# Performance work log

Measured on AMD Instinct MI355X. Metric: run time of the kernel, lower is better.

## Reference

```python
import jax, jax.numpy as jnp
import numpy as np
from jax import lax

B, S, HDIM = 4, 2048, 1024
H, D, L = 16, 64, 128
NB = S // L
EPS = 1e-8


def setup_inputs() -> dict:
    key = jax.random.key(0)
    ks = jax.random.split(key, 16)
    std = 0.02
    inp = {
        'f_in': jax.random.normal(ks[0], (B, S, HDIM), jnp.float32),
        'i_in': jax.random.normal(ks[1], (B, S, HDIM), jnp.float32),
        'z_in': jax.random.normal(ks[2], (B, S, HDIM), jnp.float32),
        'o_in': jax.random.normal(ks[3], (B, S, HDIM), jnp.float32),
        'c0': jax.random.normal(ks[4], (B, H, D), jnp.float32),
        'h0': jax.random.normal(ks[5], (B, H, D), jnp.float32),
        # weights stored (in, out) so forward is x @ W + b
        'Wf': std * jax.random.normal(ks[6], (HDIM, H * D), jnp.float32),
        'bf': jnp.zeros((H * D,), jnp.float32),
        'Wi': std * jax.random.normal(ks[7], (HDIM, H * D), jnp.float32),
        'bi': jnp.zeros((H * D,), jnp.float32),
        'Wz': std * jax.random.normal(ks[8], (HDIM, H * D), jnp.float32),
        'bz': jnp.zeros((H * D,), jnp.float32),
        'Wo': std * jax.random.normal(ks[9], (HDIM, H * D), jnp.float32),
        'bo': jnp.zeros((H * D,), jnp.float32),
        'Wp': std * jax.random.normal(ks[10], (H * D, HDIM), jnp.float32),
        'bp': jnp.zeros((HDIM,), jnp.float32),
    }
    return inp


def _to_blocks(x):
    # (B,S,H*D) -> (NB, B, H, D, L), matching torch view+permute(1,0,3,4,2)
    return jnp.transpose(x.reshape(B, NB, L, H, D), (1, 0, 3, 4, 2))


def _qlstm(f_in, i_in, z_in, o_in, c0, Wf, bf, Wi, bi, Wz, bz, Wo, bo, Wp, bp):
    fx = _to_blocks(f_in @ Wf + bf)
    ix = _to_blocks(i_in @ Wi + bi)
    zx = _to_blocks(z_in @ Wz + bz)
    ox = _to_blocks(o_in @ Wo + bo)

    f = jax.nn.sigmoid(fx + 1.0)              # (NB,B,H,D,L)
    o = jax.nn.sigmoid(ox)
    update = jax.nn.sigmoid(ix) * jnp.tanh(zx)

    kk = jnp.arange(L)[:, None]
    ll = jnp.arange(L + 1)[None, :]
    ones_mask = ll >= kk + 1                   # (L, L+1): filled with 1.0
    zeros_mask = ll >= kk + 2                  # (L, L+1): zeroed out

    def block_step(c, blk):
        fb, ob, ub = blk                       # each (B,H,D,L)
        cf = jnp.concatenate([fb, jnp.ones(fb.shape[:-1] + (1,), fb.dtype)], axis=-1)  # (B,H,D,L+1)
        Fm = jnp.broadcast_to(cf[..., None, :], fb.shape[:-1] + (L, L + 1))
        Fm = jnp.where(ones_mask, 1.0, Fm)
        # reversed log-cumsum-exp along last axis (decay products)
        Fm = jnp.exp(jnp.flip(jnp.cumsum(jnp.flip(jnp.log(Fm + EPS), -1), -1), -1)) - EPS
        Fm = jnp.where(zeros_mask, 0.0, Fm)    # (B,H,D,L,L+1)
        u = jnp.concatenate([c[..., None], ub], axis=-1)   # (B,H,D,L+1)
        cs = jnp.einsum('bhdkl,bhdl->bhdk', Fm, u)          # (B,H,D,L)
        hs = ob * jnp.tanh(cs)
        return cs[..., -1], hs

    last_c, hs = lax.scan(block_step, c0, (f, o, update))   # hs: (NB,B,H,D,L)
    last_h = hs[-1, ..., -1]
    y = jnp.transpose(hs, (1, 0, 4, 2, 3)).reshape(B, S, H * D)
    y = y @ Wp + bp                            # (B,S,HDIM)
    return y, last_c, last_h


def reference(f_in, i_in, z_in, o_in, c0, h0, Wf, bf, Wi, bi, Wz, bz, Wo, bo, Wp, bp):
    y, last_c, last_h = _qlstm(f_in, i_in, z_in, o_in, c0,
                               Wf, bf, Wi, bi, Wz, bz, Wo, bo, Wp, bp)
    return y, last_c, last_h
```

## Files before the change

### kernel.cpp

```cpp
#include <hip/hip_runtime.h>
#include <hip/hip_bf16.h>
#include <stdint.h>

constexpr int GM = 8192;
constexpr int GK = 1024;
constexpr int GN = 1024;
constexpr size_t NACT = (size_t)GM * GN;
constexpr int CHUNK = 32;
constexpr int NCHUNK = 64;
constexpr int NCH = 4096;
constexpr int NT = GK / 64;

#define DEVINL __device__ __forceinline__

typedef __attribute__((ext_vector_type(8))) short bf16x8;
typedef __attribute__((ext_vector_type(4))) float f32x4;

DEVINL float sigmoidf_(float x) { return 1.0f / (1.0f + __expf(-x)); }

DEVINL unsigned short f2bf(float x) {
  unsigned int u = __builtin_bit_cast(unsigned int, x);
  unsigned int rnd = 0x7fffu + ((u >> 16) & 1u);
  return (unsigned short)((u + rnd) >> 16);
}
DEVINL float bf2f(unsigned short u) {
  unsigned int x = ((unsigned int)u) << 16;
  return __builtin_bit_cast(float, x);
}

DEVINL void gload16(const void* g, void* l) {
  __builtin_amdgcn_global_load_lds(
      (const __attribute__((address_space(1))) unsigned int*)g,
      (__attribute__((address_space(3))) unsigned int*)l, 16, 0, 0);
}

__global__ void cvt4_kernel(const float* __restrict__ s0, const float* __restrict__ s1,
                            const float* __restrict__ s2, const float* __restrict__ s3,
                            unsigned short* __restrict__ d0, unsigned short* __restrict__ d1,
                            unsigned short* __restrict__ d2, unsigned short* __restrict__ d3,
                            int n4) {
  const float* s;
  unsigned short* d;
  switch (blockIdx.y) {
    case 0: s = s0; d = d0; break;
    case 1: s = s1; d = d1; break;
    case 2: s = s2; d = d2; break;
    default: s = s3; d = d3; break;
  }
  int stride = gridDim.x * blockDim.x;
  for (int i = blockIdx.x * blockDim.x + threadIdx.x; i < n4; i += stride) {
    float4 v = ((const float4*)s)[i];
    ushort4 o;
    o.x = f2bf(v.x); o.y = f2bf(v.y); o.z = f2bf(v.z); o.w = f2bf(v.w);
    ((ushort4*)d)[i] = o;
  }
}

struct TPtrs {
  const float* src[5];
  unsigned short* dst[5];
};

__global__ void transpose_cvt_all(TPtrs p) {
  const float* __restrict__ W = p.src[blockIdx.z];
  unsigned short* __restrict__ Wt = p.dst[blockIdx.z];
  __shared__ float tile[32][33];
  int n0 = blockIdx.x * 32, k0 = blockIdx.y * 32;
  int tx = threadIdx.x & 31, ty = threadIdx.x >> 5;
#pragma unroll
  for (int i = 0; i < 32; i += 8)
    tile[ty + i][tx] = W[(size_t)(k0 + ty + i) * GN + n0 + tx];
  __syncthreads();
#pragma unroll
  for (int i = 0; i < 32; i += 8)
    Wt[(size_t)(n0 + ty + i) * GK + k0 + tx] = f2bf(tile[tx][ty + i]);
}

DEVINL void gemm256_core(const unsigned short* __restrict__ A,
                         const unsigned short* __restrict__ W,
                         char* lds, int tid, int wave, int lane,
                         int bm, int bn, f32x4 (&acc)[8][4]) {
  const int Ah = wave >> 2;
  const int wn = (wave & 3) * 64;
  const int lrow = lane & 15;
  const int lgrp = lane >> 4;

  const char* gsrc[8];
  char* ldst[8];
  {
    const char* Ag = (const char*)A;
    const char* Wg = (const char*)W;
#pragma unroll
    for (int hh = 0; hh < 4; ++hh)
#pragma unroll
      for (int j = 0; j < 2; ++j) {
        const int lbyte = j * 8192 + tid * 16;
        const int row = lbyte >> 7;
        const int gcb = (lbyte & 127) ^ ((row & 7) << 4);
        const int i = hh * 2 + j;
        gsrc[i] = (hh < 2)
            ? Ag + (size_t)(bm * 256 + hh * 128 + row) * 2048 + gcb
            : Wg + (size_t)(bn * 256 + (hh - 2) * 128 + row) * 2048 + gcb;
        ldst[i] = lds + (hh >= 2 ? 32768 : 0) + (hh & 1) * 16384 + j * 8192 +
                  wave * 1024;
      }
  }

#pragma unroll
  for (int i = 0; i < 8; ++i) gload16(gsrc[i], ldst[i]);

  bf16x8 aF[4][2], bF[4][2];

  for (int t = 0; t < NT; ++t) {
    const int cur = t & 1;
    const int obuf = (cur ^ 1) * 65536;
    const char* Abase = lds + cur * 65536 + Ah * 16384;
    const char* Bbase = lds + cur * 65536 + 32768;
    const int nk = (t + 1 < NT) ? (t + 1) : (NT - 1);
    const size_t koff = (size_t)nk * 128;

#pragma unroll
    for (int i = 0; i < 4; ++i) gload16(gsrc[i] + koff, ldst[i] + obuf);
    asm volatile("s_waitcnt vmcnt(4)" ::: "memory");
    __builtin_amdgcn_s_barrier();
    __builtin_amdgcn_sched_barrier(0);
#pragma unroll
    for (int m = 0; m < 4; ++m)
#pragma unroll
      for (int ks = 0; ks < 2; ++ks) {
        const int r = m * 16 + lrow;
        const int cb = ks * 64 + lgrp * 16;
        aF[m][ks] = *(const bf16x8*)(Abase + r * 128 + (cb ^ ((r & 7) << 4)));
      }
#pragma unroll
    for (int n = 0; n < 2; ++n)
#pragma unroll
      for (int ks = 0; ks < 2; ++ks) {
        const int nr = wn + n * 16 + lrow;
        const int cb = ks * 64 + lgrp * 16;
        bF[n][ks] = *(const bf16x8*)(Bbase + nr * 128 + (cb ^ ((nr & 7) << 4)));
      }
    __builtin_amdgcn_s_setprio(1);
#pragma unroll
    for (int m = 0; m < 4; ++m)
#pragma unroll
      for (int n = 0; n < 2; ++n)
#pragma unroll
        for (int ks = 0; ks < 2; ++ks)
          acc[m][n] = __builtin_amdgcn_mfma_f32_16x16x32_bf16(aF[m][ks], bF[n][ks],
                                                              acc[m][n], 0, 0, 0);
    __builtin_amdgcn_s_setprio(0);

#pragma unroll
    for (int n = 2; n < 4; ++n)
#pragma unroll
      for (int ks = 0; ks < 2; ++ks) {
        const int nr = wn + n * 16 + lrow;
        const int cb = ks * 64 + lgrp * 16;
        bF[n][ks] = *(const bf16x8*)(Bbase + nr * 128 + (cb ^ ((nr & 7) << 4)));
      }
#pragma unroll
    for (int i = 4; i < 8; ++i) gload16(gsrc[i] + koff, ldst[i] + obuf);
    __builtin_amdgcn_s_barrier();
    asm volatile("s_waitcnt lgkmcnt(0)" ::: "memory");
    __builtin_amdgcn_sched_barrier(0);
    __builtin_amdgcn_s_setprio(1);
#pragma unroll
    for (int m = 0; m < 4; ++m)
#pragma unroll
      for (int n = 2; n < 4; ++n)
#pragma unroll
        for (int ks = 0; ks < 2; ++ks)
          acc[m][n] = __builtin_amdgcn_mfma_f32_16x16x32_bf16(aF[m][ks], bF[n][ks],
                                                              acc[m][n], 0, 0, 0);
    __builtin_amdgcn_s_setprio(0);

#pragma unroll
    for (int m = 0; m < 4; ++m)
#pragma unroll
      for (int ks = 0; ks < 2; ++ks) {
        const int r = (m + 4) * 16 + lrow;
        const int cb = ks * 64 + lgrp * 16;
        aF[m][ks] = *(const bf16x8*)(Abase + r * 128 + (cb ^ ((r & 7) << 4)));
      }
    __builtin_amdgcn_s_barrier();
    asm volatile("s_waitcnt lgkmcnt(0)" ::: "memory");
    __builtin_amdgcn_sched_barrier(0);
    __builtin_amdgcn_s_setprio(1);
#pragma unroll
    for (int m = 0; m < 4; ++m)
#pragma unroll
      for (int n = 2; n < 4; ++n)
#pragma unroll
        for (int ks = 0; ks < 2; ++ks)
          acc[m + 4][n] = __builtin_amdgcn_mfma_f32_16x16x32_bf16(aF[m][ks], bF[n][ks],
                                                                  acc[m + 4][n], 0, 0, 0);
    __builtin_amdgcn_s_setprio(0);

    __builtin_amdgcn_s_barrier();
    __builtin_amdgcn_s_setprio(1);
#pragma unroll
    for (int m = 0; m < 4; ++m)
#pragma unroll
      for (int n = 0; n < 2; ++n)
#pragma unroll
        for (int ks = 0; ks < 2; ++ks)
          acc[m + 4][n] = __builtin_amdgcn_mfma_f32_16x16x32_bf16(aF[m][ks], bF[n][ks],
                                                                  acc[m + 4][n], 0, 0, 0);
    __builtin_amdgcn_s_setprio(0);
  }
}

struct GateArgs {
  const unsigned short* A[4];
  const unsigned short* W[4];
  const float* bias[4];
  unsigned short* out[4];
};

__global__ __launch_bounds__(512, 2) void gemm_gates8(GateArgs ga) {
  extern __shared__ char lds[];
  const int tid = threadIdx.x;
  const int wave = tid >> 6, lane = tid & 63;
  const int bm = blockIdx.x, bn = blockIdx.y, gz = blockIdx.z;
  const int wm = (wave >> 2) * 128, wn = (wave & 3) * 64;
  const int lrow = lane & 15, lgrp = lane >> 4;

  f32x4 acc[8][4];
#pragma unroll
  for (int m = 0; m < 8; ++m)
#pragma unroll
    for (int n = 0; n < 4; ++n) acc[m][n] = (f32x4){0.f, 0.f, 0.f, 0.f};

  gemm256_core(ga.A[gz], ga.W[gz], lds, tid, wave, lane, bm, bn, acc);

  const float* bias = ga.bias[gz];
  unsigned short* out = ga.out[gz];
  float bv[4];
#pragma unroll
  for (int n = 0; n < 4; ++n) bv[n] = bias[bn * 256 + wn + n * 16 + lrow];

#pragma unroll
  for (int m = 0; m < 8; ++m)
#pragma unroll
    for (int n = 0; n < 4; ++n) {
      const int gc = bn * 256 + wn + n * 16 + lrow;
#pragma unroll
      for (int j = 0; j < 4; ++j) {
        const int gr = bm * 256 + wm + m * 16 + lgrp * 4 + j;
        float v = acc[m][n][j] + bv[n];
        if (gz == 0) v = sigmoidf_(v + 1.0f);
        else if (gz == 1) v = sigmoidf_(v);
        out[(size_t)gr * GN + gc] = f2bf(v);
      }
    }
}

__global__ __launch_bounds__(512, 2) void gemm_proj8(
    const unsigned short* __restrict__ A, const unsigned short* __restrict__ W,
    const float* __restrict__ bias, float* __restrict__ out) {
  extern __shared__ char lds[];
  const int tid = threadIdx.x;
  const int wave = tid >> 6, lane = tid & 63;
  const int bm = blockIdx.x, bn = blockIdx.y;
  const int wm = (wave >> 2) * 128, wn = (wave & 3) * 64;
  const int lrow = lane & 15, lgrp = lane >> 4;

  f32x4 acc[8][4];
#pragma unroll
  for (int m = 0; m < 8; ++m)
#pragma unroll
    for (int n = 0; n < 4; ++n) acc[m][n] = (f32x4){0.f, 0.f, 0.f, 0.f};

  gemm256_core(A, W, lds, tid, wave, lane, bm, bn, acc);

  float bv[4];
#pragma unroll
  for (int n = 0; n < 4; ++n) bv[n] = bias[bn * 256 + wn + n * 16 + lrow];

#pragma unroll
  for (int m = 0; m < 8; ++m)
#pragma unroll
    for (int n = 0; n < 4; ++n) {
      const int gc = bn * 256 + wn + n * 16 + lrow;
#pragma unroll
      for (int j = 0; j < 4; ++j) {
        const int gr = bm * 256 + wm + m * 16 + lgrp * 4 + j;
        out[(size_t)gr * GN + gc] = acc[m][n][j] + bv[n];
      }
    }
}

__global__ void scan_phaseA_kernel(const unsigned short* __restrict__ F,
                                   const unsigned short* __restrict__ Ip,
                                   const unsigned short* __restrict__ Zp,
                                   float* __restrict__ Pt, float* __restrict__ Ct) {
  int tid = blockIdx.x * blockDim.x + threadIdx.x;
  int ch = tid & (NCH - 1), chunk = tid >> 12;
  int b = ch >> 10, n = ch & 1023;
  size_t base = ((size_t)(b * 2048 + chunk * CHUNK)) * 1024 + n;
  float c = 0.f, P = 1.f;
#pragma unroll 8
  for (int t = 0; t < CHUNK; ++t) {
    size_t idx = base + (size_t)t * 1024;
    float f = bf2f(F[idx]);
    float u = sigmoidf_(bf2f(Ip[idx])) * tanhf(bf2f(Zp[idx]));
    c = __builtin_fmaf(f, c, u);
    P *= f;
  }
  Pt[tid] = P;
  Ct[tid] = c;
}

__global__ void scan_combine_kernel(const float* __restrict__ Pt,
                                    const float* __restrict__ Ct,
                                    const float* __restrict__ c0,
                                    float* __restrict__ Cin,
                                    float* __restrict__ last_c) {
  int ch = blockIdx.x * blockDim.x + threadIdx.x;
  float c = c0[ch];
#pragma unroll
  for (int j = 0; j < NCHUNK; ++j) {
    Cin[j * NCH + ch] = c;
    c = __builtin_fmaf(Pt[j * NCH + ch], c, Ct[j * NCH + ch]);
  }
  last_c[ch] = c;
}

__global__ void scan_phaseC_kernel(const unsigned short* __restrict__ F,
                                   const unsigned short* __restrict__ Ip,
                                   const unsigned short* __restrict__ Zp,
                                   const unsigned short* __restrict__ O,
                                   const float* __restrict__ Cin,
                                   unsigned short* __restrict__ Hb,
                                   float* __restrict__ last_h) {
  int tid = blockIdx.x * blockDim.x + threadIdx.x;
  int ch = tid & (NCH - 1), chunk = tid >> 12;
  int b = ch >> 10, n = ch & 1023;
  size_t base = ((size_t)(b * 2048 + chunk * CHUNK)) * 1024 + n;
  float c = Cin[tid];
  float h = 0.f;
#pragma unroll 8
  for (int t = 0; t < CHUNK; ++t) {
    size_t idx = base + (size_t)t * 1024;
    float f = bf2f(F[idx]);
    float u = sigmoidf_(bf2f(Ip[idx])) * tanhf(bf2f(Zp[idx]));
    float o = bf2f(O[idx]);
    c = __builtin_fmaf(f, c, u);
    h = o * tanhf(c);
    Hb[idx] = f2bf(h);
  }
  if (chunk == NCHUNK - 1) last_h[ch] = h;
}

extern "C" void kernel_launch(void* const* d_in, const int* in_sizes, int n_in,
                              void* d_out, int out_size, void* d_ws, size_t ws_size,
                              hipStream_t stream) {
  const float* f_in = (const float*)d_in[0];
  const float* i_in = (const float*)d_in[1];
  const float* z_in = (const float*)d_in[2];
  const float* o_in = (const float*)d_in[3];
  const float* c0 = (const float*)d_in[4];
  const float* Wf = (const float*)d_in[6];
  const float* bf_ = (const float*)d_in[7];
  const float* Wi = (const float*)d_in[8];
  const float* bi = (const float*)d_in[9];
  const float* Wz = (const float*)d_in[10];
  const float* bz = (const float*)d_in[11];
  const float* Wo = (const float*)d_in[12];
  const float* bo = (const float*)d_in[13];
  const float* Wp = (const float*)d_in[14];
  const float* bp = (const float*)d_in[15];

  float* y = (float*)d_out;
  float* last_c = y + NACT;
  float* last_h = last_c + NCH;

  char* w = (char*)d_ws;
  const size_t ABYTES = NACT * 2;
  const size_t WBYTES = (size_t)GK * GN * 2;
  unsigned short* Af = (unsigned short*)(w + 0 * ABYTES);
  unsigned short* Ai = (unsigned short*)(w + 1 * ABYTES);
  unsigned short* Az = (unsigned short*)(w + 2 * ABYTES);
  unsigned short* Ao = (unsigned short*)(w + 3 * ABYTES);
  char* wt = w + 4 * ABYTES;
  unsigned short* Wtf = (unsigned short*)(wt + 0 * WBYTES);
  unsigned short* Wti = (unsigned short*)(wt + 1 * WBYTES);
  unsigned short* Wtz = (unsigned short*)(wt + 2 * WBYTES);
  unsigned short* Wto = (unsigned short*)(wt + 3 * WBYTES);
  unsigned short* Wtp = (unsigned short*)(wt + 4 * WBYTES);
  char* gp = wt + 5 * WBYTES;
  unsigned short* F = (unsigned short*)(gp + 0 * ABYTES);
  unsigned short* O = (unsigned short*)(gp + 1 * ABYTES);
  unsigned short* Ip = (unsigned short*)(gp + 2 * ABYTES);
  unsigned short* Zp = (unsigned short*)(gp + 3 * ABYTES);
  unsigned short* Hb = Af;
  char* sp = gp + 4 * ABYTES;
  const size_t SBYTES = (size_t)NCH * NCHUNK * 4;
  float* Pt = (float*)(sp + 0 * SBYTES);
  float* Ct = (float*)(sp + 1 * SBYTES);
  float* Cin = (float*)(sp + 2 * SBYTES);

  (void)hipFuncSetAttribute((const void*)gemm_gates8,
                            hipFuncAttributeMaxDynamicSharedMemorySize, 131072);
  (void)hipFuncSetAttribute((const void*)gemm_proj8,
                            hipFuncAttributeMaxDynamicSharedMemorySize, 131072);

  cvt4_kernel<<<dim3(1024, 4), 256, 0, stream>>>(
      f_in, o_in, i_in, z_in, Af, Ao, Ai, Az, (int)(NACT / 4));

  TPtrs tp;
  tp.src[0] = Wf; tp.src[1] = Wi; tp.src[2] = Wz; tp.src[3] = Wo; tp.src[4] = Wp;
  tp.dst[0] = Wtf; tp.dst[1] = Wti; tp.dst[2] = Wtz; tp.dst[3] = Wto; tp.dst[4] = Wtp;
  transpose_cvt_all<<<dim3(32, 32, 5), 256, 0, stream>>>(tp);

  GateArgs ga;
  ga.A[0] = Af;  ga.A[1] = Ao;  ga.A[2] = Ai;  ga.A[3] = Az;
  ga.W[0] = Wtf; ga.W[1] = Wto; ga.W[2] = Wti; ga.W[3] = Wtz;
  ga.bias[0] = bf_; ga.bias[1] = bo; ga.bias[2] = bi; ga.bias[3] = bz;
  ga.out[0] = F; ga.out[1] = O; ga.out[2] = Ip; ga.out[3] = Zp;
  gemm_gates8<<<dim3(GM / 256, GN / 256, 4), 512, 131072, stream>>>(ga);

  scan_phaseA_kernel<<<(NCH * NCHUNK) / 256, 256, 0, stream>>>(F, Ip, Zp, Pt, Ct);
  scan_combine_kernel<<<NCH / 256, 256, 0, stream>>>(Pt, Ct, c0, Cin, last_c);
  scan_phaseC_kernel<<<(NCH * NCHUNK) / 256, 256, 0, stream>>>(F, Ip, Zp, O, Cin, Hb,
                                                               last_h);

  gemm_proj8<<<dim3(GM / 256, GN / 256), 512, 131072, stream>>>(Hb, Wtp, bp, y);
}
```

Measured before the change: 206.1 us.

## Restructure GEMM mainloop with full fragment registers and one barrier per k-step

Changes the GEMM inner loop from four barrier-separated phases with shared fragment registers to a single barrier per k-tile. All eight async global-to-LDS loads for the next tile are issued right after it. All A/B fragments for the tile are held in separate Lo/Hi registers, with partial lgkmcnt waits so the MFMAs can start while later LDS reads are still in flight. This cuts barrier overhead and lets LDS reads overlap with MFMA work. In exchange it raises register pressure and waits on vmcnt(0), which may expose global load latency at the top of each iteration.

```diff
diff --git a/kernel.cpp b/kernel.cpp
--- a/kernel.cpp
+++ b/kernel.cpp
@@ -33,6 +33,8 @@
       (const __attribute__((address_space(1))) unsigned int*)g,
       (__attribute__((address_space(3))) unsigned int*)l, 16, 0, 0);
 }
+
+#define SB() __builtin_amdgcn_sched_barrier(0)
 
 __global__ void cvt4_kernel(const float* __restrict__ s0, const float* __restrict__ s1,
                             const float* __restrict__ s2, const float* __restrict__ s3,
@@ -109,7 +111,7 @@
 #pragma unroll
   for (int i = 0; i < 8; ++i) gload16(gsrc[i], ldst[i]);
 
-  bf16x8 aF[4][2], bF[4][2];
+  bf16x8 aLo[4][2], aHi[4][2], bLo[2][2], bHi[2][2];
 
   for (int t = 0; t < NT; ++t) {
     const int cur = t & 1;
@@ -119,18 +121,21 @@
     const int nk = (t + 1 < NT) ? (t + 1) : (NT - 1);
     const size_t koff = (size_t)nk * 128;
 
-#pragma unroll
-    for (int i = 0; i < 4; ++i) gload16(gsrc[i] + koff, ldst[i] + obuf);
-    asm volatile("s_waitcnt vmcnt(4)" ::: "memory");
+    asm volatile("s_waitcnt vmcnt(0)" ::: "memory");
+    SB();
     __builtin_amdgcn_s_barrier();
-    __builtin_amdgcn_sched_barrier(0);
+    SB();
+
+#pragma unroll
+    for (int i = 0; i < 8; ++i) gload16(gsrc[i] + koff, ldst[i] + obuf);
+
 #pragma unroll
     for (int m = 0; m < 4; ++m)
 #pragma unroll
       for (int ks = 0; ks < 2; ++ks) {
         const int r = m * 16 + lrow;
         const int cb = ks * 64 + lgrp * 16;
-        aF[m][ks] = *(const bf16x8*)(Abase + r * 128 + (cb ^ ((r & 7) << 4)));
+        aLo[m][ks] = *(const bf16x8*)(Abase + r * 128 + (cb ^ ((r & 7) << 4)));
       }
 #pragma unroll
     for (int n = 0; n < 2; ++n)
@@ -138,75 +143,70 @@
       for (int ks = 0; ks < 2; ++ks) {
         const int nr = wn + n * 16 + lrow;
         const int cb = ks * 64 + lgrp * 16;
-        bF[n][ks] = *(const bf16x8*)(Bbase + nr * 128 + (cb ^ ((nr & 7) << 4)));
-      }
-    __builtin_amdgcn_s_setprio(1);
-#pragma unroll
-    for (int m = 0; m < 4; ++m)
-#pragma unroll
-      for (int n = 0; n < 2; ++n)
-#pragma unroll
-        for (int ks = 0; ks < 2; ++ks)
-          acc[m][n] = __builtin_amdgcn_mfma_f32_16x16x32_bf16(aF[m][ks], bF[n][ks],
-                                                              acc[m][n], 0, 0, 0);
-    __builtin_amdgcn_s_setprio(0);
-
-#pragma unroll
-    for (int n = 2; n < 4; ++n)
+        bLo[n][ks] = *(const bf16x8*)(Bbase + nr * 128 + (cb ^ ((nr & 7) << 4)));
+      }
+    asm volatile("s_waitcnt lgkmcnt(4)" ::: "memory");
+    SB();
+#pragma unroll
+    for (int n = 0; n < 2; ++n)
 #pragma unroll
       for (int ks = 0; ks < 2; ++ks) {
-        const int nr = wn + n * 16 + lrow;
+        const int nr = wn + (n + 2) * 16 + lrow;
         const int cb = ks * 64 + lgrp * 16;
-        bF[n][ks] = *(const bf16x8*)(Bbase + nr * 128 + (cb ^ ((nr & 7) << 4)));
-      }
-#pragma unroll
-    for (int i = 4; i < 8; ++i) gload16(gsrc[i] + koff, ldst[i] + obuf);
-    __builtin_amdgcn_s_barrier();
-    asm volatile("s_waitcnt lgkmcnt(0)" ::: "memory");
-    __builtin_amdgcn_sched_barrier(0);
-    __builtin_amdgcn_s_setprio(1);
-#pragma unroll
-    for (int m = 0; m < 4; ++m)
-#pragma unroll
-      for (int n = 2; n < 4; ++n)
-#pragma unroll
-        for (int ks = 0; ks < 2; ++ks)
-          acc[m][n] = __builtin_amdgcn_mfma_f32_16x16x32_bf16(aF[m][ks], bF[n][ks],
-                                                              acc[m][n], 0, 0, 0);
-    __builtin_amdgcn_s_setprio(0);
-
+        bHi[n][ks] = *(const bf16x8*)(Bbase + nr * 128 + (cb ^ ((nr & 7) << 4)));
+      }
+    asm volatile("s_waitcnt lgkmcnt(4)" ::: "memory");
+    SB();
 #pragma unroll
     for (int m = 0; m < 4; ++m)
 #pragma unroll
       for (int ks = 0; ks < 2; ++ks) {
         const int r = (m + 4) * 16 + lrow;
         const int cb = ks * 64 + lgrp * 16;
-        aF[m][ks] = *(const bf16x8*)(Abase + r * 128 + (cb ^ ((r & 7) << 4)));
-      }
-    __builtin_amdgcn_s_barrier();
+        aHi[m][ks] = *(const bf16x8*)(Abase + r * 128 + (cb ^ ((r & 7) << 4)));
+      }
+
+    __builtin_amdgcn_s_setprio(1);
+#pragma unroll
+    for (int m = 0; m < 4; ++m)
+#pragma unroll
+      for (int n = 0; n < 2; ++n)
+#pragma unroll
+        for (int ks = 0; ks < 2; ++ks)
+          acc[m][n] = __builtin_amdgcn_mfma_f32_16x16x32_bf16(aLo[m][ks], bLo[n][ks],
+                                                              acc[m][n], 0, 0, 0);
+    __builtin_amdgcn_s_setprio(0);
+    asm volatile("s_waitcnt lgkmcnt(8)" ::: "memory");
+    SB();
+    __builtin_amdgcn_s_setprio(1);
+#pragma unroll
+    for (int m = 0; m < 4; ++m)
+#pragma unroll
+      for (int n = 0; n < 2; ++n)
+#pragma unroll
+        for (int ks = 0; ks < 2; ++ks)
+          acc[m][n + 2] = __builtin_amdgcn_mfma_f32_16x16x32_bf16(aLo[m][ks], bHi[n][ks],
+                                                                  acc[m][n + 2], 0, 0, 0);
+    __builtin_amdgcn_s_setprio(0);
     asm volatile("s_waitcnt lgkmcnt(0)" ::: "memory");
-    __builtin_amdgcn_sched_barrier(0);
+    SB();
     __builtin_amdgcn_s_setprio(1);
 #pragma unroll
     for (int m = 0; m < 4; ++m)
 #pragma unroll
-      for (int n = 2; n < 4; ++n)
+      for (int n = 0; n < 2; ++n)
 #pragma unroll
         for (int ks = 0; ks < 2; ++ks)
-          acc[m + 4][n] = __builtin_amdgcn_mfma_f32_16x16x32_bf16(aF[m][ks], bF[n][ks],
-                                                                  acc[m + 4][n], 0, 0, 0);
-    __builtin_amdgcn_s_setprio(0);
-
-    __builtin_amdgcn_s_barrier();
-    __builtin_amdgcn_s_setprio(1);
+          acc[m + 4][n + 2] = __builtin_amdgcn_mfma_f32_16x16x32_bf16(
+              aHi[m][ks], bHi[n][ks], acc[m + 4][n + 2], 0, 0, 0);
 #pragma unroll
     for (int m = 0; m < 4; ++m)
 #pragma unroll
       for (int n = 0; n < 2; ++n)
 #pragma unroll
         for (int ks = 0; ks < 2; ++ks)
-          acc[m + 4][n] = __builtin_amdgcn_mfma_f32_16x16x32_bf16(aF[m][ks], bF[n][ks],
-                                                                  acc[m + 4][n], 0, 0, 0);
+          acc[m + 4][n] = __builtin_amdgcn_mfma_f32_16x16x32_bf16(
+              aHi[m][ks], bLo[n][ks], acc[m + 4][n], 0, 0, 0);
     __builtin_amdgcn_s_setprio(0);
   }
 }
```

Result: slower. 211.0 us (+2.4%).
